# Kernel tuning notes

Hardware: AMD Instinct MI355X
Metric: run time of the kernel (lower is better)

## Reference

```python
import jax, jax.numpy as jnp
import numpy as np

NEG_INF = -1e9  # additive mask value for masked softmax


def setup_inputs() -> dict:
    key = jax.random.key(0)
    k1, k2, k3, k4, k5 = jax.random.split(key, 5)
    bz, rv_num, rv_len, in_feat, out_feat = 32, 10, 128, 300, 128
    seq_a = jax.random.normal(k1, (bz, rv_num, rv_len, in_feat), dtype=jnp.float32)
    seq_b = jax.random.normal(k2, (bz, rv_num, rv_len, in_feat), dtype=jnp.float32)
    mask_a = jax.random.randint(k3, (bz, rv_num, rv_len), 0, 2, dtype=jnp.int32)
    mask_b = jax.random.randint(k4, (bz, rv_num, rv_len), 0, 2, dtype=jnp.int32)
    # guarantee at least one valid position per review (avoid fully-masked rows)
    mask_a = mask_a.at[:, :, 0].set(1)
    mask_b = mask_b.at[:, :, 0].set(1)
    # FC transform params (xavier-normal-ish weight, zero bias)
    W = jax.random.normal(k5, (in_feat, out_feat), dtype=jnp.float32) * (2.0 / np.sqrt(in_feat + out_feat))
    b = jnp.zeros((out_feat,), dtype=jnp.float32)
    return {"seq_a": seq_a, "seq_b": seq_b, "mask_a": mask_a, "mask_b": mask_b, "W": W, "b": b}


def _masked_softmax(scores, mask):
    # scores: [N, L], mask: [N, L] in {0,1}
    logits = jnp.where(mask > 0, scores, NEG_INF)
    return jax.nn.softmax(logits, axis=-1)


def reference(seq_a, seq_b, mask_a, mask_b, W, b):
    bz, rv_num, rv_len, _ = seq_a.shape
    hdim = W.shape[1]
    N = bz * rv_num          # flattened batch of reviews
    M = rv_num * rv_len      # all tokens on the other side

    # FC + ReLU feature transform
    ta = jax.nn.relu(jnp.einsum('bnld,dh->bnlh', seq_a, W) + b)
    tb = jax.nn.relu(jnp.einsum('bnld,dh->bnlh', seq_b, W) + b)

    sa = ta.reshape(N, rv_len, hdim)
    sb = tb.reshape(N, rv_len, hdim)
    # expand: each review attends over ALL tokens of the other sequence in its sample
    ea = jnp.broadcast_to(ta.reshape(bz, 1, M, hdim), (bz, rv_num, M, hdim)).reshape(N, M, hdim)
    eb = jnp.broadcast_to(tb.reshape(bz, 1, M, hdim), (bz, rv_num, M, hdim)).reshape(N, M, hdim)

    # DOT interaction (no scale): affinity [N, rv_len, M]
    atob_aff = jnp.einsum('nld,nmd->nlm', sa, eb)
    btoa_aff = jnp.einsum('nld,nmd->nlm', sb, ea)

    # MEAN pooling over the other-sequence axis
    atob_scores = atob_aff.mean(axis=-1)  # [N, rv_len]
    btoa_scores = btoa_aff.mean(axis=-1)

    ma = mask_a.reshape(N, rv_len)
    mb = mask_b.reshape(N, rv_len)
    atob_w = _masked_softmax(atob_scores, ma)
    btoa_w = _masked_softmax(btoa_scores, mb)

    a_out = jnp.einsum('nl,nld->nd', atob_w, sa)
    b_out = jnp.einsum('nl,nld->nd', btoa_w, sb)
    return (a_out, b_out, atob_w, btoa_w)
```

## Files before the change

### kernel.cpp

```cpp
#include <hip/hip_runtime.h>
#include <hip/hip_bf16.h>


#define K_FEAT 300
#define KP 320
#define H 128
#define NTOK 40960
#define NREV 320
#define TOK_PER_SAMPLE 1280
#define TM 64
#define BLKS_PER_SAMPLE (TOK_PER_SAMPLE / TM)
#define LDA 40

typedef __attribute__((ext_vector_type(8))) short bf16x8;
typedef __attribute__((ext_vector_type(4))) float f32x4;

static __device__ __forceinline__ unsigned short f2bf(float x) {
    unsigned int u = __float_as_uint(x);
    unsigned int r = (u + 0x7fffu + ((u >> 16) & 1u)) >> 16;
    return (unsigned short)r;
}
static __device__ __forceinline__ float bf2f(unsigned short s) {
    return __uint_as_float(((unsigned int)s) << 16);
}

__global__ void wsplit_kernel(const float* __restrict__ W,
                              unsigned short* __restrict__ Wh_t,
                              unsigned short* __restrict__ Wl_t)
{
    int i = blockIdx.x * 256 + threadIdx.x;
    if (i >= H * KP) return;
    int h = i / KP;
    int k = i - h * KP;
    float w = (k < K_FEAT) ? W[(size_t)k * H + h] : 0.f;
    unsigned short hi = f2bf(w);
    unsigned short lo = f2bf(w - bf2f(hi));
    Wh_t[h * KP + k] = hi;
    Wl_t[h * KP + k] = lo;
}

__global__ __launch_bounds__(256, 4) void fc_mfma_kernel(
    const float* __restrict__ seq_a, const float* __restrict__ seq_b,
    const unsigned short* __restrict__ Wh_t, const unsigned short* __restrict__ Wl_t,
    const float* __restrict__ bias,
    float* __restrict__ ta, float* __restrict__ tb,
    float* __restrict__ psum_a, float* __restrict__ psum_b)
{
    __shared__ unsigned short Ah_s[TM * LDA];
    __shared__ unsigned short Al_s[TM * LDA];
    __shared__ unsigned short Wh_s[H * LDA];
    __shared__ unsigned short Wl_s[H * LDA];
    __shared__ float bias_s[H];
    __shared__ float psum_s[H];

    int blk = blockIdx.x;
    const float* seq;
    float* outp;
    float* psum;
    if (blk < 640) { seq = seq_a; outp = ta; psum = psum_a; }
    else           { seq = seq_b; outp = tb; psum = psum_b; blk -= 640; }

    const int tid = threadIdx.x;
    const int tok0 = blk * TM;
    const int wave = tid >> 6;
    const int lane = tid & 63;
    const int nn = lane & 15;
    const int quad = lane >> 4;

    if (tid < H) { bias_s[tid] = bias[tid]; psum_s[tid] = 0.f; }

    f32x4 acc[8];
#pragma unroll
    for (int nt = 0; nt < 8; ++nt) acc[nt] = (f32x4){0.f, 0.f, 0.f, 0.f};

    for (int c = 0; c < 10; ++c) {
        int k0 = c * 32;
        __syncthreads();
#pragma unroll
        for (int it = 0; it < 2; ++it) {
            int i = tid + it * 256;
            int t = i >> 3;
            int j = i & 7;
            int kk = k0 + 4 * j;
            float4 v = make_float4(0.f, 0.f, 0.f, 0.f);
            if (kk + 3 < K_FEAT)
                v = *(const float4*)&seq[(size_t)(tok0 + t) * K_FEAT + kk];
            unsigned short h0 = f2bf(v.x), h1 = f2bf(v.y), h2 = f2bf(v.z), h3 = f2bf(v.w);
            uint2 hp, lp;
            hp.x = (unsigned)h0 | ((unsigned)h1 << 16);
            hp.y = (unsigned)h2 | ((unsigned)h3 << 16);
            lp.x = (unsigned)f2bf(v.x - bf2f(h0)) | ((unsigned)f2bf(v.y - bf2f(h1)) << 16);
            lp.y = (unsigned)f2bf(v.z - bf2f(h2)) | ((unsigned)f2bf(v.w - bf2f(h3)) << 16);
            *(uint2*)&Ah_s[t * LDA + 4 * j] = hp;
            *(uint2*)&Al_s[t * LDA + 4 * j] = lp;
        }
#pragma unroll
        for (int it = 0; it < 2; ++it) {
            int i = tid + it * 256;
            int h = i >> 2;
            int j = i & 3;
            uint4 vh = *(const uint4*)&Wh_t[h * KP + k0 + 8 * j];
            uint4 vl = *(const uint4*)&Wl_t[h * KP + k0 + 8 * j];
            *(uint4*)&Wh_s[h * LDA + 8 * j] = vh;
            *(uint4*)&Wl_s[h * LDA + 8 * j] = vl;
        }
        __syncthreads();

        bf16x8 a_hi = *(const bf16x8*)&Ah_s[(wave * 16 + nn) * LDA + quad * 8];
        bf16x8 a_lo = *(const bf16x8*)&Al_s[(wave * 16 + nn) * LDA + quad * 8];
#pragma unroll
        for (int nt = 0; nt < 8; ++nt) {
            bf16x8 b_hi = *(const bf16x8*)&Wh_s[(nt * 16 + nn) * LDA + quad * 8];
            bf16x8 b_lo = *(const bf16x8*)&Wl_s[(nt * 16 + nn) * LDA + quad * 8];
            acc[nt] = __builtin_amdgcn_mfma_f32_16x16x32_bf16(a_hi, b_hi, acc[nt], 0, 0, 0);
            acc[nt] = __builtin_amdgcn_mfma_f32_16x16x32_bf16(a_hi, b_lo, acc[nt], 0, 0, 0);
            acc[nt] = __builtin_amdgcn_mfma_f32_16x16x32_bf16(a_lo, b_hi, acc[nt], 0, 0, 0);
        }
    }

#pragma unroll
    for (int nt = 0; nt < 8; ++nt) {
        int hcol = nt * 16 + nn;
        float bv = bias_s[hcol];
        float rsum = 0.f;
#pragma unroll
        for (int reg = 0; reg < 4; ++reg) {
            int tok = tok0 + wave * 16 + quad * 4 + reg;
            float v = fmaxf(acc[nt][reg] + bv, 0.f);
            outp[(size_t)tok * H + hcol] = v;
            rsum += v;
        }
        rsum += __shfl_xor(rsum, 16);
        rsum += __shfl_xor(rsum, 32);
        if (quad == 0) atomicAdd(&psum_s[hcol], rsum);
    }
    __syncthreads();
    if (tid < H) psum[(size_t)blk * H + tid] = psum_s[tid];
}

__global__ __launch_bounds__(256) void attn_kernel(
    const float* __restrict__ ta, const float* __restrict__ tb,
    const int* __restrict__ mask_a, const int* __restrict__ mask_b,
    const float* __restrict__ psum_a, const float* __restrict__ psum_b,
    float* __restrict__ out)
{
    int n = blockIdx.x;
    int side = 0;
    if (n >= NREV) { side = 1; n -= NREV; }

    const float* t = side ? tb : ta;
    const int* mask = side ? mask_b : mask_a;
    const float* psum_o = side ? psum_a : psum_b;
    float* out_vec = out + (side ? NREV * H : 0);
    float* out_w = out + 2 * NREV * H + (side ? NREV * H : 0);

    int sample = n / 10;
    int tid = threadIdx.x;

    __shared__ float score_part[128 * 33];
    __shared__ float mean_s[128];
    __shared__ float w_s[128];
    __shared__ float red[4];
    __shared__ float part_out[8 * 128];

    if (tid < 128) {
        float s = 0.f;
        const float* pb = psum_o + (size_t)sample * BLKS_PER_SAMPLE * H + tid;
#pragma unroll
        for (int i = 0; i < BLKS_PER_SAMPLE; ++i) s += pb[(size_t)i * H];
        mean_s[tid] = s * (1.0f / (float)TOK_PER_SAMPLE);
    }
    __syncthreads();

    const float* rowbase = t + (size_t)n * 128 * H;

#pragma unroll
    for (int i = 0; i < 16; ++i) {
        int q = tid + 256 * i;
        int r = q >> 5;
        int c4 = q & 31;
        float4 v = *(const float4*)&rowbase[q * 4];
        float4 m = *(const float4*)&mean_s[c4 * 4];
        score_part[r * 33 + c4] = v.x * m.x + v.y * m.y + v.z * m.z + v.w * m.w;
    }
    __syncthreads();

    float logit = -1e9f;
    if (tid < 128) {
        float s = 0.f;
#pragma unroll
        for (int j = 0; j < 32; ++j) s += score_part[tid * 33 + j];
        int mv = mask[n * 128 + tid];
        logit = (mv > 0) ? s : -1e9f;
    }

    float mx = logit;
    for (int off = 32; off > 0; off >>= 1) mx = fmaxf(mx, __shfl_xor(mx, off));
    if ((tid & 63) == 0) red[tid >> 6] = mx;
    __syncthreads();
    mx = fmaxf(fmaxf(red[0], red[1]), fmaxf(red[2], red[3]));
    __syncthreads();

    float e = __expf(logit - mx);
    float ssum = e;
    for (int off = 32; off > 0; off >>= 1) ssum += __shfl_xor(ssum, off);
    if ((tid & 63) == 0) red[tid >> 6] = ssum;
    __syncthreads();
    ssum = red[0] + red[1] + red[2] + red[3];

    float w = e / ssum;
    if (tid < 128) {
        w_s[tid] = w;
        out_w[n * 128 + tid] = w;
    }
    __syncthreads();

    int c4 = tid & 31;
    int lp = tid >> 5;
    float4 o4 = make_float4(0.f, 0.f, 0.f, 0.f);
#pragma unroll
    for (int k = 0; k < 16; ++k) {
        int l = k * 8 + lp;
        float wl = w_s[l];
        float4 v = *(const float4*)&rowbase[(size_t)l * H + c4 * 4];
        o4.x = fmaf(wl, v.x, o4.x);
        o4.y = fmaf(wl, v.y, o4.y);
        o4.z = fmaf(wl, v.z, o4.z);
        o4.w = fmaf(wl, v.w, o4.w);
    }
    *(float4*)&part_out[lp * 128 + c4 * 4] = o4;
    __syncthreads();
    if (tid < 128) {
        float o = 0.f;
#pragma unroll
        for (int p = 0; p < 8; ++p) o += part_out[p * 128 + tid];
        out_vec[n * 128 + tid] = o;
    }
}

extern "C" void kernel_launch(void* const* d_in, const int* in_sizes, int n_in,
                              void* d_out, int out_size, void* d_ws, size_t ws_size,
                              hipStream_t stream)
{
    const float* seq_a = (const float*)d_in[0];
    const float* seq_b = (const float*)d_in[1];
    const int* mask_a = (const int*)d_in[2];
    const int* mask_b = (const int*)d_in[3];
    const float* W = (const float*)d_in[4];
    const float* bias = (const float*)d_in[5];
    float* out = (float*)d_out;

    float* ws = (float*)d_ws;
    float* ta = ws;
    float* tb = ta + (size_t)NTOK * H;
    float* psum_a = tb + (size_t)NTOK * H;
    float* psum_b = psum_a + 640 * H;
    unsigned short* Wh_t = (unsigned short*)(psum_b + 640 * H);
    unsigned short* Wl_t = Wh_t + H * KP;

    wsplit_kernel<<<(H * KP + 255) / 256, 256, 0, stream>>>(W, Wh_t, Wl_t);
    fc_mfma_kernel<<<1280, 256, 0, stream>>>(seq_a, seq_b, Wh_t, Wl_t, bias,
                                             ta, tb, psum_a, psum_b);
    attn_kernel<<<640, 256, 0, stream>>>(ta, tb, mask_a, mask_b, psum_a, psum_b, out);
}
```

Baseline: 169.2 us.

## Enlarge FC token tile to 128 and pre-chunk split weights for contiguous LDS loads

Doubles the token tile per FC block and reassigns each wave to two output-column tiles across all 128 tokens, so weight fragments are held in registers and reused over eight MFMA row tiles. The hi/lo bf16 weight split is precomputed in a chunked, padded layout that is copied straight into LDS. Per-block column sums are written directly instead of through shared atomics. This halves the number of blocks and raises register and LDS use per block, which lowers occupancy.

```diff
diff --git a/kernel.cpp b/kernel.cpp
--- a/kernel.cpp
+++ b/kernel.cpp
@@ -3,62 +3,60 @@
 
 
 #define K_FEAT 300
-#define KP 320
 #define H 128
 #define NTOK 40960
 #define NREV 320
 #define TOK_PER_SAMPLE 1280
-#define TM 64
-#define BLKS_PER_SAMPLE (TOK_PER_SAMPLE / TM)
+#define TM 128
+#define BLKS_PER_SAMPLE 10
 #define LDA 40
+#define NCHUNK 10
+#define WCHUNK (2 * H * LDA)
 
 typedef __attribute__((ext_vector_type(8))) short bf16x8;
 typedef __attribute__((ext_vector_type(4))) float f32x4;
-
-static __device__ __forceinline__ unsigned short f2bf(float x) {
-    unsigned int u = __float_as_uint(x);
-    unsigned int r = (u + 0x7fffu + ((u >> 16) & 1u)) >> 16;
-    return (unsigned short)r;
-}
-static __device__ __forceinline__ float bf2f(unsigned short s) {
-    return __uint_as_float(((unsigned int)s) << 16);
-}
-
-__global__ void wsplit_kernel(const float* __restrict__ W,
-                              unsigned short* __restrict__ Wh_t,
-                              unsigned short* __restrict__ Wl_t)
+typedef unsigned short u16;
+typedef unsigned int u32;
+
+static __device__ __forceinline__ u16 f2bf(float x) {
+    u32 u = __float_as_uint(x);
+    return (u16)((u + 0x7fffu + ((u >> 16) & 1u)) >> 16);
+}
+static __device__ __forceinline__ float bf2f(u16 s) {
+    return __uint_as_float(((u32)s) << 16);
+}
+
+__global__ void wsplit_kernel(const float* __restrict__ W, u16* __restrict__ Wc)
 {
     int i = blockIdx.x * 256 + threadIdx.x;
-    if (i >= H * KP) return;
-    int h = i / KP;
-    int k = i - h * KP;
-    float w = (k < K_FEAT) ? W[(size_t)k * H + h] : 0.f;
-    unsigned short hi = f2bf(w);
-    unsigned short lo = f2bf(w - bf2f(hi));
-    Wh_t[h * KP + k] = hi;
-    Wl_t[h * KP + k] = lo;
-}
-
-__global__ __launch_bounds__(256, 4) void fc_mfma_kernel(
+    if (i >= NCHUNK * WCHUNK) return;
+    int c = i / WCHUNK;
+    int rem = i - c * WCHUNK;
+    int part = rem / (H * LDA);
+    int rem2 = rem - part * (H * LDA);
+    int h = rem2 / LDA;
+    int kk = rem2 - h * LDA;
+    int k = c * 32 + kk;
+    float w = (kk < 32 && k < K_FEAT) ? W[(size_t)k * H + h] : 0.f;
+    u16 hi = f2bf(w);
+    Wc[i] = part ? f2bf(w - bf2f(hi)) : hi;
+}
+
+__global__ __launch_bounds__(256, 3) void fc_mfma_kernel(
     const float* __restrict__ seq_a, const float* __restrict__ seq_b,
-    const unsigned short* __restrict__ Wh_t, const unsigned short* __restrict__ Wl_t,
-    const float* __restrict__ bias,
+    const u16* __restrict__ Wc, const float* __restrict__ bias,
     float* __restrict__ ta, float* __restrict__ tb,
     float* __restrict__ psum_a, float* __restrict__ psum_b)
 {
-    __shared__ unsigned short Ah_s[TM * LDA];
-    __shared__ unsigned short Al_s[TM * LDA];
-    __shared__ unsigned short Wh_s[H * LDA];
-    __shared__ unsigned short Wl_s[H * LDA];
+    __shared__ u16 Ah_s[TM * LDA];
+    __shared__ u16 Al_s[TM * LDA];
+    __shared__ u16 W_s[WCHUNK];
     __shared__ float bias_s[H];
-    __shared__ float psum_s[H];
 
     int blk = blockIdx.x;
-    const float* seq;
-    float* outp;
-    float* psum;
-    if (blk < 640) { seq = seq_a; outp = ta; psum = psum_a; }
-    else           { seq = seq_b; outp = tb; psum = psum_b; blk -= 640; }
+    const float* seq; float* outp; float* psum;
+    if (blk < 320) { seq = seq_a; outp = ta; psum = psum_a; }
+    else           { seq = seq_b; outp = tb; psum = psum_b; blk -= 320; }
 
     const int tid = threadIdx.x;
     const int tok0 = blk * TM;
@@ -67,75 +65,79 @@
     const int nn = lane & 15;
     const int quad = lane >> 4;
 
-    if (tid < H) { bias_s[tid] = bias[tid]; psum_s[tid] = 0.f; }
-
-    f32x4 acc[8];
-#pragma unroll
-    for (int nt = 0; nt < 8; ++nt) acc[nt] = (f32x4){0.f, 0.f, 0.f, 0.f};
-
-    for (int c = 0; c < 10; ++c) {
-        int k0 = c * 32;
+    if (tid < H) bias_s[tid] = bias[tid];
+
+    f32x4 acc[8][2];
+#pragma unroll
+    for (int m = 0; m < 8; ++m) {
+        acc[m][0] = (f32x4){0.f, 0.f, 0.f, 0.f};
+        acc[m][1] = (f32x4){0.f, 0.f, 0.f, 0.f};
+    }
+
+    for (int c = 0; c < NCHUNK; ++c) {
         __syncthreads();
 #pragma unroll
-        for (int it = 0; it < 2; ++it) {
+        for (int it = 0; it < 4; ++it) {
             int i = tid + it * 256;
             int t = i >> 3;
             int j = i & 7;
-            int kk = k0 + 4 * j;
+            int kk = c * 32 + 4 * j;
             float4 v = make_float4(0.f, 0.f, 0.f, 0.f);
-            if (kk + 3 < K_FEAT)
+            if (kk + 4 <= K_FEAT)
                 v = *(const float4*)&seq[(size_t)(tok0 + t) * K_FEAT + kk];
-            unsigned short h0 = f2bf(v.x), h1 = f2bf(v.y), h2 = f2bf(v.z), h3 = f2bf(v.w);
+            u16 h0 = f2bf(v.x), h1 = f2bf(v.y), h2 = f2bf(v.z), h3 = f2bf(v.w);
             uint2 hp, lp;
-            hp.x = (unsigned)h0 | ((unsigned)h1 << 16);
-            hp.y = (unsigned)h2 | ((unsigned)h3 << 16);
-            lp.x = (unsigned)f2bf(v.x - bf2f(h0)) | ((unsigned)f2bf(v.y - bf2f(h1)) << 16);
-            lp.y = (unsigned)f2bf(v.z - bf2f(h2)) | ((unsigned)f2bf(v.w - bf2f(h3)) << 16);
+            hp.x = (u32)h0 | ((u32)h1 << 16);
+            hp.y = (u32)h2 | ((u32)h3 << 16);
+            lp.x = (u32)f2bf(v.x - bf2f(h0)) | ((u32)f2bf(v.y - bf2f(h1)) << 16);
+            lp.y = (u32)f2bf(v.z - bf2f(h2)) | ((u32)f2bf(v.w - bf2f(h3)) << 16);
             *(uint2*)&Ah_s[t * LDA + 4 * j] = hp;
             *(uint2*)&Al_s[t * LDA + 4 * j] = lp;
         }
-#pragma unroll
-        for (int it = 0; it < 2; ++it) {
+        const u16* wsrc = Wc + (size_t)c * WCHUNK;
+#pragma unroll
+        for (int it = 0; it < 5; ++it) {
             int i = tid + it * 256;
-            int h = i >> 2;
-            int j = i & 3;
-            uint4 vh = *(const uint4*)&Wh_t[h * KP + k0 + 8 * j];
-            uint4 vl = *(const uint4*)&Wl_t[h * KP + k0 + 8 * j];
-            *(uint4*)&Wh_s[h * LDA + 8 * j] = vh;
-            *(uint4*)&Wl_s[h * LDA + 8 * j] = vl;
+            *(uint4*)&W_s[i * 8] = *(const uint4*)&wsrc[i * 8];
         }
         __syncthreads();
 
-        bf16x8 a_hi = *(const bf16x8*)&Ah_s[(wave * 16 + nn) * LDA + quad * 8];
-        bf16x8 a_lo = *(const bf16x8*)&Al_s[(wave * 16 + nn) * LDA + quad * 8];
-#pragma unroll
-        for (int nt = 0; nt < 8; ++nt) {
-            bf16x8 b_hi = *(const bf16x8*)&Wh_s[(nt * 16 + nn) * LDA + quad * 8];
-            bf16x8 b_lo = *(const bf16x8*)&Wl_s[(nt * 16 + nn) * LDA + quad * 8];
-            acc[nt] = __builtin_amdgcn_mfma_f32_16x16x32_bf16(a_hi, b_hi, acc[nt], 0, 0, 0);
-            acc[nt] = __builtin_amdgcn_mfma_f32_16x16x32_bf16(a_hi, b_lo, acc[nt], 0, 0, 0);
-            acc[nt] = __builtin_amdgcn_mfma_f32_16x16x32_bf16(a_lo, b_hi, acc[nt], 0, 0, 0);
-        }
-    }
-
-#pragma unroll
-    for (int nt = 0; nt < 8; ++nt) {
-        int hcol = nt * 16 + nn;
+        bf16x8 bh0 = *(const bf16x8*)&W_s[((2 * wave + 0) * 16 + nn) * LDA + quad * 8];
+        bf16x8 bl0 = *(const bf16x8*)&W_s[5120 + ((2 * wave + 0) * 16 + nn) * LDA + quad * 8];
+        bf16x8 bh1 = *(const bf16x8*)&W_s[((2 * wave + 1) * 16 + nn) * LDA + quad * 8];
+        bf16x8 bl1 = *(const bf16x8*)&W_s[5120 + ((2 * wave + 1) * 16 + nn) * LDA + quad * 8];
+#pragma unroll
+        for (int m = 0; m < 8; ++m) {
+            bf16x8 a_hi = *(const bf16x8*)&Ah_s[(m * 16 + nn) * LDA + quad * 8];
+            bf16x8 a_lo = *(const bf16x8*)&Al_s[(m * 16 + nn) * LDA + quad * 8];
+            acc[m][0] = __builtin_amdgcn_mfma_f32_16x16x32_bf16(a_hi, bh0, acc[m][0], 0, 0, 0);
+            acc[m][0] = __builtin_amdgcn_mfma_f32_16x16x32_bf16(a_hi, bl0, acc[m][0], 0, 0, 0);
+            acc[m][0] = __builtin_amdgcn_mfma_f32_16x16x32_bf16(a_lo, bh0, acc[m][0], 0, 0, 0);
+            acc[m][1] = __builtin_amdgcn_mfma_f32_16x16x32_bf16(a_hi, bh1, acc[m][1], 0, 0, 0);
+            acc[m][1] = __builtin_amdgcn_mfma_f32_16x16x32_bf16(a_hi, bl1, acc[m][1], 0, 0, 0);
+            acc[m][1] = __builtin_amdgcn_mfma_f32_16x16x32_bf16(a_lo, bh1, acc[m][1], 0, 0, 0);
+        }
+    }
+
+#pragma unroll
+    for (int t2 = 0; t2 < 2; ++t2) {
+        int hcol = (2 * wave + t2) * 16 + nn;
         float bv = bias_s[hcol];
-        float rsum = 0.f;
-#pragma unroll
-        for (int reg = 0; reg < 4; ++reg) {
-            int tok = tok0 + wave * 16 + quad * 4 + reg;
-            float v = fmaxf(acc[nt][reg] + bv, 0.f);
-            outp[(size_t)tok * H + hcol] = v;
-            rsum += v;
-        }
-        rsum += __shfl_xor(rsum, 16);
-        rsum += __shfl_xor(rsum, 32);
-        if (quad == 0) atomicAdd(&psum_s[hcol], rsum);
-    }
-    __syncthreads();
-    if (tid < H) psum[(size_t)blk * H + tid] = psum_s[tid];
+        float fs = 0.f;
+#pragma unroll
+        for (int m = 0; m < 8; ++m) {
+#pragma unroll
+            for (int reg = 0; reg < 4; ++reg) {
+                int tok = tok0 + m * 16 + quad * 4 + reg;
+                float v = fmaxf(acc[m][t2][reg] + bv, 0.f);
+                outp[(size_t)tok * H + hcol] = v;
+                fs += v;
+            }
+        }
+        fs += __shfl_xor(fs, 16);
+        fs += __shfl_xor(fs, 32);
+        if (quad == 0) psum[(size_t)blk * H + hcol] = fs;
+    }
 }
 
 __global__ __launch_bounds__(256) void attn_kernel(
@@ -254,12 +256,10 @@
     float* ta = ws;
     float* tb = ta + (size_t)NTOK * H;
     float* psum_a = tb + (size_t)NTOK * H;
-    float* psum_b = psum_a + 640 * H;
-    unsigned short* Wh_t = (unsigned short*)(psum_b + 640 * H);
-    unsigned short* Wl_t = Wh_t + H * KP;
-
-    wsplit_kernel<<<(H * KP + 255) / 256, 256, 0, stream>>>(W, Wh_t, Wl_t);
-    fc_mfma_kernel<<<1280, 256, 0, stream>>>(seq_a, seq_b, Wh_t, Wl_t, bias,
-                                             ta, tb, psum_a, psum_b);
+    float* psum_b = psum_a + NREV * H;
+    u16* Wc = (u16*)(psum_b + NREV * H);
+
+    wsplit_kernel<<<(NCHUNK * WCHUNK + 255) / 256, 256, 0, stream>>>(W, Wc);
+    fc_mfma_kernel<<<640, 256, 0, stream>>>(seq_a, seq_b, Wc, bias, ta, tb, psum_a, psum_b);
     attn_kernel<<<640, 256, 0, stream>>>(ta, tb, mask_a, mask_b, psum_a, psum_b, out);
 }
```

New measurement: 169.6 us. About the same (+0.2%).
